# Kernel tuning notes

Hardware: AMD Instinct MI355X
Metric: run time of the kernel (lower is better)

Reference implementation:

```python
import jax, jax.numpy as jnp
import numpy as np

TEMP = 0.05
EPS = 1e-6


def _l2norm(x):
    return x / jnp.linalg.norm(x, axis=1, keepdims=True)


def setup_inputs() -> dict:
    key = jax.random.key(0)
    k1, k2, k3, k4 = jax.random.split(key, 4)
    B, D = 4096, 768
    return {
        "feat": jax.random.normal(k1, (B, D), dtype=jnp.float32),
        "feat_gen": jax.random.normal(k2, (B, D), dtype=jnp.float32),
        "feat_aug": jax.random.normal(k3, (B, D), dtype=jnp.float32),
        "targets": jax.random.randint(k4, (B,), 0, 100, dtype=jnp.int64),
    }


def reference(feat, feat_gen, feat_aug, targets):
    B = feat.shape[0]
    on = _l2norm(feat)
    gn = _l2norm(feat_gen)
    an = _l2norm(feat_aug)
    # [B, B] exp-similarity matrices
    exp_ori = jnp.exp(on @ on.T / TEMP)
    exp_gen = jnp.exp(on @ gn.T / TEMP)
    exp_aug = jnp.exp(on @ an.T / TEMP)

    same = (targets[:, None] == targets[None, :])  # [B, B] bool, includes diagonal
    same_f = same.astype(exp_ori.dtype)

    # ---- co loss: anchors vs ori+aug columns ----
    oa = exp_ori + exp_aug
    diff_sum_oa = oa.sum(axis=1) - (oa * same_f).sum(axis=1)        # [B]
    denom_co = diff_sum_oa + exp_gen.sum(axis=1) + EPS              # [B]
    term_o = -jnp.log(exp_ori / (exp_ori + denom_co[:, None]) + EPS)
    term_a = -jnp.log(exp_aug / (exp_aug + denom_co[:, None]) + EPS)
    co_loss = ((term_o + term_a) * same_f).sum() / B

    # ---- ad loss: anchors vs gen columns ----
    diff_sum_g = exp_gen.sum(axis=1) - (exp_gen * same_f).sum(axis=1)
    denom_ad = diff_sum_g + exp_aug.sum(axis=1) + exp_ori.sum(axis=1) + EPS
    term_g = -jnp.log(exp_gen / (exp_gen + denom_ad[:, None]) + EPS)
    ad_loss = (term_g * same_f).sum() / B

    return (ad_loss, co_loss)
```

## Files before the change

### kernel.cpp

```cpp
#include <hip/hip_runtime.h>
#include <hip/hip_bf16.h>
#include <math.h>

#define Bn 4096
#define Dd 768
#define SC2 28.85390081777927f
#define EPSF 1e-6f
#define DG 4.8516519541e8f

#define O_S      0
#define O_SMOA   12288
#define O_SMG    16384
#define ZERO_F   20480
#define O_P      20480
#define O_RM     20608
#define LIST_OFF   262144
#define LCAP       (1u << 19)
#define NB_OFF     33554432

typedef __attribute__((ext_vector_type(8))) short sh8;
typedef __attribute__((ext_vector_type(4))) float f32x4;

#define AS1 __attribute__((address_space(1)))
#define AS3 __attribute__((address_space(3)))

static __device__ __forceinline__ void gl_lds16(const void* g, void* l) {
    __builtin_amdgcn_global_load_lds((const AS1 void*)g, (AS3 void*)l, 16, 0, 0);
}

static __device__ __forceinline__ unsigned short f2b(float f) {
    unsigned int u = __float_as_uint(f);
    unsigned int r = (u + 0x7fffu + ((u >> 16) & 1u)) >> 16;
    return (unsigned short)r;
}

__global__ void norm_kernel(const float* f0, const float* f1, const float* f2, unsigned short* nb) {
    int r = blockIdx.x, m = blockIdx.y, tid = threadIdx.x;
    const float* src = (m == 0 ? f0 : (m == 1 ? f1 : f2)) + (size_t)r * Dd;
    float x0 = src[tid], x1 = src[tid + 256], x2 = src[tid + 512];
    float v = x0 * x0 + x1 * x1 + x2 * x2;
    #pragma unroll
    for (int off = 1; off < 64; off <<= 1) v += __shfl_xor(v, off);
    __shared__ float wr[4];
    if ((tid & 63) == 0) wr[tid >> 6] = v;
    __syncthreads();
    float inv = rsqrtf(wr[0] + wr[1] + wr[2] + wr[3]);
    unsigned short* dst = nb + ((size_t)m * Bn + r) * Dd;
    dst[tid] = f2b(x0 * inv);
    dst[tid + 256] = f2b(x1 * inv);
    dst[tid + 512] = f2b(x2 * inv);
}

__launch_bounds__(1024)
__global__ void sort_kernel(const int* tg, unsigned int* I, float* out) {
    float* F = (float*)I;
    __shared__ unsigned int h[128], pb[128], cur[128];
    int tid = threadIdx.x;
    for (int e = tid; e < ZERO_F; e += 1024) F[e] = 0.f;
    if (tid == 0) { out[0] = 0.f; out[1] = 0.f; }
    if (tid < 128) { h[tid] = 0; cur[tid] = 0; }
    __syncthreads();
    for (int e = tid; e < Bn; e += 1024) atomicAdd(&h[tg[e]], 1u);
    __syncthreads();
    if (tid < 128) pb[tid] = h[tid] * h[tid];
    __syncthreads();
    for (int s = 1; s < 128; s <<= 1) {
        unsigned int b = 0;
        if (tid < 128 && tid >= s) b = pb[tid - s];
        __syncthreads();
        if (tid < 128) pb[tid] += b;
        __syncthreads();
    }
    if (tid == 127) I[O_P] = pb[127];
    uint2* RM = (uint2*)(I + O_RM);
    for (int e = tid; e < Bn; e += 1024) {
        int c = tg[e];
        unsigned int r = atomicAdd(&cur[c], 1u);
        unsigned int n = h[c];
        RM[e] = make_uint2((unsigned)c | (r << 8), (pb[c] - n * n) + r * n);
    }
}

__launch_bounds__(256, 2)
__global__ void gemm_rowsum(const unsigned short* nb, char* ws) {
    float* F = (float*)ws;
    const unsigned int* I = (const unsigned int*)ws;
    const uint2* RM = (const uint2*)(I + O_RM);
    int bid = blockIdx.x;
    int sw = (bid & 7) * 128 + (bid >> 3);
    int m0 = (sw >> 5) * 128, n0 = (sw & 31) * 128;
    int tid = threadIdx.x, lane = tid & 63, wave = tid >> 6;
    int wm = (wave >> 1) * 64, wn = (wave & 1) * 64;
    int lid = lane & 15, q = lane >> 4;
    __shared__ __align__(16) unsigned short Asm[128 * 32];
    __shared__ __align__(16) unsigned short Bsm[3][128 * 32];

    int row0 = tid >> 2, ch = tid & 3;
    int cs = (ch ^ ((row0 >> 1) & 3)) * 8;
    const unsigned short* gA  = nb + (size_t)(m0 + row0) * Dd + cs;
    const unsigned short* gB0 = nb + (size_t)(n0 + row0) * Dd + cs;
    const unsigned short* gB1 = gB0 + (size_t)Bn * Dd;
    const unsigned short* gB2 = gB1 + (size_t)Bn * Dd;
    unsigned short* lA0 = &Asm[tid * 8];
    unsigned short* lA1 = &Asm[(tid + 256) * 8];

    int cswz = (q ^ ((lid >> 1) & 3)) * 8;

    f32x4 a0[4][4] = {}, a1[4][4] = {}, a2[4][4] = {};

    for (int kt = 0; kt < 24; ++kt) {
        const unsigned short* pa  = gA  + kt * 32;
        const unsigned short* pb0 = gB0 + kt * 32;
        const unsigned short* pb1 = gB1 + kt * 32;
        const unsigned short* pb2 = gB2 + kt * 32;
        __syncthreads();
        gl_lds16(pa, lA0);
        gl_lds16(pa + (size_t)64 * Dd, lA1);
        gl_lds16(pb0, &Bsm[0][tid * 8]);
        gl_lds16(pb0 + (size_t)64 * Dd, &Bsm[0][(tid + 256) * 8]);
        gl_lds16(pb1, &Bsm[1][tid * 8]);
        gl_lds16(pb1 + (size_t)64 * Dd, &Bsm[1][(tid + 256) * 8]);
        gl_lds16(pb2, &Bsm[2][tid * 8]);
        gl_lds16(pb2 + (size_t)64 * Dd, &Bsm[2][(tid + 256) * 8]);
        __syncthreads();
        sh8 af[4];
        #pragma unroll
        for (int i = 0; i < 4; ++i)
            af[i] = *(const sh8*)&Asm[(wm + i * 16 + lid) * 32 + cswz];
        {
            sh8 bf[4];
            #pragma unroll
            for (int j = 0; j < 4; ++j)
                bf[j] = *(const sh8*)&Bsm[0][(wn + j * 16 + lid) * 32 + cswz];
            #pragma unroll
            for (int i = 0; i < 4; ++i)
                #pragma unroll
                for (int j = 0; j < 4; ++j)
                    a0[i][j] = __builtin_amdgcn_mfma_f32_16x16x32_bf16(af[i], bf[j], a0[i][j], 0, 0, 0);
        }
        {
            sh8 bf[4];
            #pragma unroll
            for (int j = 0; j < 4; ++j)
                bf[j] = *(const sh8*)&Bsm[1][(wn + j * 16 + lid) * 32 + cswz];
            #pragma unroll
            for (int i = 0; i < 4; ++i)
                #pragma unroll
                for (int j = 0; j < 4; ++j)
                    a1[i][j] = __builtin_amdgcn_mfma_f32_16x16x32_bf16(af[i], bf[j], a1[i][j], 0, 0, 0);
        }
        {
            sh8 bf[4];
            #pragma unroll
            for (int j = 0; j < 4; ++j)
                bf[j] = *(const sh8*)&Bsm[2][(wn + j * 16 + lid) * 32 + cswz];
            #pragma unroll
            for (int i = 0; i < 4; ++i)
                #pragma unroll
                for (int j = 0; j < 4; ++j)
                    a2[i][j] = __builtin_amdgcn_mfma_f32_16x16x32_bf16(af[i], bf[j], a2[i][j], 0, 0, 0);
        }
    }

    uint2 rmc[4];
    #pragma unroll
    for (int j = 0; j < 4; ++j) rmc[j] = RM[n0 + wn + j * 16 + lid];
    uint4* Lq = (uint4*)(ws + LIST_OFF);
    #pragma unroll
    for (int i = 0; i < 4; ++i)
        #pragma unroll
        for (int reg = 0; reg < 4; ++reg) {
            int grow = m0 + wm + i * 16 + q * 4 + reg;
            uint2 rm = RM[grow];
            unsigned int trow = rm.x & 255u, rsb = rm.y;
            float rs0 = 0.f, rs1 = 0.f, rs2 = 0.f, msOA = 0.f, msG = 0.f;
            #pragma unroll
            for (int j = 0; j < 4; ++j) {
                int gcol = n0 + wn + j * 16 + lid;
                float x0 = a0[i][j][reg] * SC2;
                float x1 = a1[i][j][reg] * SC2;
                float x2 = a2[i][j][reg] * SC2;
                float e0 = exp2f(x0);
                float e1 = exp2f(x1);
                float e2 = exp2f(x2);
                if (gcol == grow) e0 = 0.f;
                rs0 += e0; rs1 += e1; rs2 += e2;
                if ((rmc[j].x & 255u) == trow) {
                    msOA += e0 + e2;
                    msG  += e1;
                    unsigned int slot = rsb + (rmc[j].x >> 8);
                    if (slot < LCAP)
                        Lq[slot] = make_uint4((unsigned)grow, __float_as_uint(x0),
                                              __float_as_uint(x1), __float_as_uint(x2));
                }
            }
            #pragma unroll
            for (int off = 1; off < 16; off <<= 1) {
                rs0 += __shfl_xor(rs0, off);
                rs1 += __shfl_xor(rs1, off);
                rs2 += __shfl_xor(rs2, off);
                msOA += __shfl_xor(msOA, off);
                msG  += __shfl_xor(msG, off);
            }
            if (lid == 0) {
                atomicAdd(&F[O_S + grow], rs0);
                atomicAdd(&F[O_S + Bn + grow], rs1);
                atomicAdd(&F[O_S + 2 * Bn + grow], rs2);
                atomicAdd(&F[O_SMOA + grow], msOA);
                atomicAdd(&F[O_SMG + grow], msG);
            }
        }
}

__launch_bounds__(256)
__global__ void loss_kernel(char* ws, float* out) {
    float* F = (float*)ws;
    const unsigned int* I = (const unsigned int*)ws;
    const uint4* L = (const uint4*)(ws + LIST_OFF);
    unsigned int n = I[O_P]; if (n > LCAP) n = LCAP;
    float a0 = 0.f, a1 = 0.f;
    unsigned int stride = gridDim.x * 256;
    for (unsigned int idx = blockIdx.x * 256 + threadIdx.x; idx < n; idx += stride) {
        uint4 en = L[idx];
        int i = (int)en.x;
        float son = F[O_S + i], sgen = F[O_S + Bn + i], saug = F[O_S + 2 * Bn + i];
        float dco = (son + saug - F[O_SMOA + i]) + sgen + EPSF;
        float dad = (sgen - F[O_SMG + i]) + saug + son + DG + EPSF;
        float eo = exp2f(__uint_as_float(en.y));
        float eg = exp2f(__uint_as_float(en.z));
        float ea = exp2f(__uint_as_float(en.w));
        a0 += -__logf(eg / (eg + dad) + EPSF);
        a1 += -__logf(eo / (eo + dco) + EPSF) - __logf(ea / (ea + dco) + EPSF);
    }
    #pragma unroll
    for (int off = 1; off < 64; off <<= 1) { a0 += __shfl_xor(a0, off); a1 += __shfl_xor(a1, off); }
    __shared__ float r0[4], r1[4];
    int tid = threadIdx.x;
    if ((tid & 63) == 0) { r0[tid >> 6] = a0; r1[tid >> 6] = a1; }
    __syncthreads();
    if (tid == 0) {
        atomicAdd(&out[0], (r0[0] + r0[1] + r0[2] + r0[3]) * (1.0f / Bn));
        atomicAdd(&out[1], (r1[0] + r1[1] + r1[2] + r1[3]) * (1.0f / Bn));
    }
}

extern "C" void kernel_launch(void* const* d_in, const int* in_sizes, int n_in,
                              void* d_out, int out_size, void* d_ws, size_t ws_size,
                              hipStream_t stream) {
    const float* f0 = (const float*)d_in[0];
    const float* f1 = (const float*)d_in[1];
    const float* f2 = (const float*)d_in[2];
    const int* tg = (const int*)d_in[3];
    char* ws = (char*)d_ws;
    unsigned int* I = (unsigned int*)d_ws;
    unsigned short* nb = (unsigned short*)(ws + NB_OFF);
    float* out = (float*)d_out;

    norm_kernel<<<dim3(Bn, 3), 256, 0, stream>>>(f0, f1, f2, nb);
    sort_kernel<<<1, 1024, 0, stream>>>(tg, I, out);
    gemm_rowsum<<<dim3(1024), 256, 0, stream>>>(nb, ws);
    loss_kernel<<<256, 256, 0, stream>>>(ws, out);
}
```

Measured before the change: 205.4 us.

## Triple-buffer LDS tiles with prefetch depth two and MFMA priority hints

Replaces the single-buffered LDS load/compute loop in the fused GEMM with a three-stage ring. Tiles for k-steps kt+1 and kt+2 are fetched asynchronously while step kt is computed, using explicit vmcnt waits and one barrier per iteration. It also raises wave priority around the MFMA blocks. The goal is to hide global-to-LDS latency that was fully exposed between the two syncthreads. LDS use grows from 32KB to 96KB per block, which may cut occupancy below the two blocks per CU the launch bounds request.

```diff
diff --git a/kernel.cpp b/kernel.cpp
--- a/kernel.cpp
+++ b/kernel.cpp
@@ -80,6 +80,8 @@
         RM[e] = make_uint2((unsigned)c | (r << 8), (pb[c] - n * n) + r * n);
     }
 }
+
+#define BUFS 16384
 
 __launch_bounds__(256, 2)
 __global__ void gemm_rowsum(const unsigned short* nb, char* ws) {
@@ -92,8 +94,7 @@
     int tid = threadIdx.x, lane = tid & 63, wave = tid >> 6;
     int wm = (wave >> 1) * 64, wn = (wave & 1) * 64;
     int lid = lane & 15, q = lane >> 4;
-    __shared__ __align__(16) unsigned short Asm[128 * 32];
-    __shared__ __align__(16) unsigned short Bsm[3][128 * 32];
+    __shared__ __align__(16) unsigned short L[3 * BUFS];
 
     int row0 = tid >> 2, ch = tid & 3;
     int cs = (ch ^ ((row0 >> 1) & 3)) * 8;
@@ -101,65 +102,85 @@
     const unsigned short* gB0 = nb + (size_t)(n0 + row0) * Dd + cs;
     const unsigned short* gB1 = gB0 + (size_t)Bn * Dd;
     const unsigned short* gB2 = gB1 + (size_t)Bn * Dd;
-    unsigned short* lA0 = &Asm[tid * 8];
-    unsigned short* lA1 = &Asm[(tid + 256) * 8];
 
     int cswz = (q ^ ((lid >> 1) & 3)) * 8;
 
     f32x4 a0[4][4] = {}, a1[4][4] = {}, a2[4][4] = {};
 
+#define STAGE(b, kt) { \
+    const unsigned short* pa  = gA  + (kt) * 32; \
+    const unsigned short* pb0 = gB0 + (kt) * 32; \
+    const unsigned short* pb1 = gB1 + (kt) * 32; \
+    const unsigned short* pb2 = gB2 + (kt) * 32; \
+    unsigned short* Lb = &L[(b) * BUFS]; \
+    gl_lds16(pa, &Lb[tid * 8]); \
+    gl_lds16(pa + (size_t)64 * Dd, &Lb[(tid + 256) * 8]); \
+    gl_lds16(pb0, &Lb[4096 + tid * 8]); \
+    gl_lds16(pb0 + (size_t)64 * Dd, &Lb[4096 + (tid + 256) * 8]); \
+    gl_lds16(pb1, &Lb[8192 + tid * 8]); \
+    gl_lds16(pb1 + (size_t)64 * Dd, &Lb[8192 + (tid + 256) * 8]); \
+    gl_lds16(pb2, &Lb[12288 + tid * 8]); \
+    gl_lds16(pb2 + (size_t)64 * Dd, &Lb[12288 + (tid + 256) * 8]); \
+}
+#define RAWBAR { __builtin_amdgcn_sched_barrier(0); __builtin_amdgcn_s_barrier(); __builtin_amdgcn_sched_barrier(0); }
+
+    STAGE(0, 0);
+    STAGE(1, 1);
+    asm volatile("s_waitcnt vmcnt(8)" ::: "memory");
+    RAWBAR;
+
+    int bc = 0, bs = 2;
     for (int kt = 0; kt < 24; ++kt) {
-        const unsigned short* pa  = gA  + kt * 32;
-        const unsigned short* pb0 = gB0 + kt * 32;
-        const unsigned short* pb1 = gB1 + kt * 32;
-        const unsigned short* pb2 = gB2 + kt * 32;
-        __syncthreads();
-        gl_lds16(pa, lA0);
-        gl_lds16(pa + (size_t)64 * Dd, lA1);
-        gl_lds16(pb0, &Bsm[0][tid * 8]);
-        gl_lds16(pb0 + (size_t)64 * Dd, &Bsm[0][(tid + 256) * 8]);
-        gl_lds16(pb1, &Bsm[1][tid * 8]);
-        gl_lds16(pb1 + (size_t)64 * Dd, &Bsm[1][(tid + 256) * 8]);
-        gl_lds16(pb2, &Bsm[2][tid * 8]);
-        gl_lds16(pb2 + (size_t)64 * Dd, &Bsm[2][(tid + 256) * 8]);
-        __syncthreads();
+        if (kt < 22) STAGE(bs, kt + 2);
+        const unsigned short* Lc = &L[bc * BUFS];
         sh8 af[4];
         #pragma unroll
         for (int i = 0; i < 4; ++i)
-            af[i] = *(const sh8*)&Asm[(wm + i * 16 + lid) * 32 + cswz];
+            af[i] = *(const sh8*)&Lc[(wm + i * 16 + lid) * 32 + cswz];
         {
             sh8 bf[4];
             #pragma unroll
             for (int j = 0; j < 4; ++j)
-                bf[j] = *(const sh8*)&Bsm[0][(wn + j * 16 + lid) * 32 + cswz];
+                bf[j] = *(const sh8*)&Lc[4096 + (wn + j * 16 + lid) * 32 + cswz];
+            __builtin_amdgcn_s_setprio(1);
             #pragma unroll
             for (int i = 0; i < 4; ++i)
                 #pragma unroll
                 for (int j = 0; j < 4; ++j)
                     a0[i][j] = __builtin_amdgcn_mfma_f32_16x16x32_bf16(af[i], bf[j], a0[i][j], 0, 0, 0);
+            __builtin_amdgcn_s_setprio(0);
         }
         {
             sh8 bf[4];
             #pragma unroll
             for (int j = 0; j < 4; ++j)
-                bf[j] = *(const sh8*)&Bsm[1][(wn + j * 16 + lid) * 32 + cswz];
+                bf[j] = *(const sh8*)&Lc[8192 + (wn + j * 16 + lid) * 32 + cswz];
+            __builtin_amdgcn_s_setprio(1);
             #pragma unroll
             for (int i = 0; i < 4; ++i)
                 #pragma unroll
                 for (int j = 0; j < 4; ++j)
                     a1[i][j] = __builtin_amdgcn_mfma_f32_16x16x32_bf16(af[i], bf[j], a1[i][j], 0, 0, 0);
+            __builtin_amdgcn_s_setprio(0);
         }
         {
             sh8 bf[4];
             #pragma unroll
             for (int j = 0; j < 4; ++j)
-                bf[j] = *(const sh8*)&Bsm[2][(wn + j * 16 + lid) * 32 + cswz];
+                bf[j] = *(const sh8*)&Lc[12288 + (wn + j * 16 + lid) * 32 + cswz];
+            __builtin_amdgcn_s_setprio(1);
             #pragma unroll
             for (int i = 0; i < 4; ++i)
                 #pragma unroll
                 for (int j = 0; j < 4; ++j)
                     a2[i][j] = __builtin_amdgcn_mfma_f32_16x16x32_bf16(af[i], bf[j], a2[i][j], 0, 0, 0);
-        }
+            __builtin_amdgcn_s_setprio(0);
+        }
+        if (kt < 22)       { asm volatile("s_waitcnt vmcnt(8)" ::: "memory"); }
+        else if (kt == 22) { asm volatile("s_waitcnt vmcnt(0)" ::: "memory"); }
+        if (kt < 23) RAWBAR;
+        bc = (bc == 2) ? 0 : bc + 1;
+        bs = (bs == 2) ? 0 : bs + 1;
     }
 
     uint2 rmc[4];
```

Result: slower. 250.0 us (+21.7%).
